# Kernel optimization log

Hardware: AMD Instinct MI355X
Metric: run time of the kernel (lower is better)

Reference implementation:

```python
import jax, jax.numpy as jnp
import numpy as np

NUM_HEADS = 16

def setup_inputs() -> dict:
    key = jax.random.key(0)
    ks = jax.random.split(key, 6)
    d_in, d_out = 1024, 1024
    x = jax.random.normal(ks[0], (4, 2048, d_in), dtype=jnp.float32)
    s = 0.02
    Wq = jax.random.normal(ks[1], (d_in, d_out), dtype=jnp.float32) * s
    Wk = jax.random.normal(ks[2], (d_in, d_out), dtype=jnp.float32) * s
    Wv = jax.random.normal(ks[3], (d_in, d_out), dtype=jnp.float32) * s
    Wo = jax.random.normal(ks[4], (d_out, d_out), dtype=jnp.float32) * s
    bo = jnp.zeros((d_out,), dtype=jnp.float32)
    return {"x": x, "Wq": Wq, "Wk": Wk, "Wv": Wv, "Wo": Wo, "bo": bo}

def reference(x, Wq, Wk, Wv, Wo, bo):
    b, n, _ = x.shape
    h = NUM_HEADS
    hd = Wq.shape[1] // h
    # project and split heads: [b, h, n, hd]
    def split(t):
        return t.reshape(b, n, h, hd).transpose(0, 2, 1, 3)
    q = split(x @ Wq)
    k = split(x @ Wk)
    v = split(x @ Wv)
    scores = jnp.einsum('bhqd,bhkd->bhqk', q, k)
    causal = jnp.tril(jnp.ones((n, n), dtype=bool))  # True = keep
    scores = jnp.where(causal, scores, -jnp.inf)
    att = jax.nn.softmax(scores / jnp.sqrt(jnp.float32(hd)), axis=-1)
    out = jnp.einsum('bhqk,bhkd->bhqd', att, v)
    out = out.transpose(0, 2, 1, 3).reshape(b, n, h * hd)
    return out @ Wo + bo
```

## Files before the change

kernel.cpp:

```cpp
#include <hip/hip_runtime.h>
#include <math.h>

namespace {
constexpr int NB = 4;
constexpr int NS = 2048;
constexpr int DM = 1024;
constexpr int NH = 16;
constexpr int DH = 64;
constexpr int M  = NB * NS;

typedef __bf16 bf16x8 __attribute__((ext_vector_type(8)));
typedef float  floatx4 __attribute__((ext_vector_type(4)));

__device__ __forceinline__ ushort f2bf(float f) {
    uint u = __float_as_uint(f);
    return (ushort)((u + 0x7FFFu + ((u >> 16) & 1u)) >> 16);
}
__device__ __forceinline__ uint cvt_pk_bf16(float lo, float hi) {
    uint r;
    asm("v_cvt_pk_bf16_f32 %0, %1, %2" : "=v"(r) : "v"(lo), "v"(hi));
    return r;
}
__device__ __forceinline__ void gload16(const void* g, void* l) {
    __builtin_amdgcn_global_load_lds(
        (const __attribute__((address_space(1))) unsigned int*)g,
        (__attribute__((address_space(3))) unsigned int*)l, 16, 0, 0);
}

__global__ __launch_bounds__(256) void conv_x_k(const float* __restrict__ in,
                                                ushort* __restrict__ out) {
    int i = blockIdx.x * 256 + threadIdx.x;
    float4 v = ((const float4*)in)[i];
    ushort4 o;
    o.x = f2bf(v.x); o.y = f2bf(v.y); o.z = f2bf(v.z); o.w = f2bf(v.w);
    ((ushort4*)out)[i] = o;
}

__global__ __launch_bounds__(256) void conv_wt4_k(const float* __restrict__ W0,
                                                  const float* __restrict__ W1,
                                                  const float* __restrict__ W2,
                                                  const float* __restrict__ W3,
                                                  ushort* __restrict__ T0,
                                                  ushort* __restrict__ T1,
                                                  ushort* __restrict__ T2,
                                                  ushort* __restrict__ T3) {
    __shared__ float tile[64][65];
    const int z = blockIdx.z;
    const float* W = (z == 0) ? W0 : (z == 1) ? W1 : (z == 2) ? W2 : W3;
    ushort* Wt     = (z == 0) ? T0 : (z == 1) ? T1 : (z == 2) ? T2 : T3;
    const int t = threadIdx.x;
    const int k0 = blockIdx.y * 64, n0 = blockIdx.x * 64;
    #pragma unroll
    for (int i = 0; i < 16; ++i) {
        int idx = i * 256 + t, r = idx >> 6, c = idx & 63;
        tile[r][c] = W[(size_t)(k0 + r) * DM + n0 + c];
    }
    __syncthreads();
    #pragma unroll
    for (int i = 0; i < 16; ++i) {
        int idx = i * 256 + t, r = idx >> 6, c = idx & 63;
        Wt[(size_t)(n0 + r) * DM + k0 + c] = f2bf(tile[c][r]);
    }
}

template<int MODE>
__global__ __launch_bounds__(512) void mm_bf16_k(const ushort* __restrict__ A,
                                                 const ushort* __restrict__ Bt,
                                                 const float* __restrict__ bias,
                                                 void* __restrict__ outp,
                                                 float oscale) {
    __shared__ __align__(16) ushort As[2 * 128 * 32];
    __shared__ __align__(16) ushort Bs[2 * 128 * 32];
    const int t  = threadIdx.x;
    const int l  = t & 63;
    const int w  = t >> 6;
    const int wr = w >> 2, wc = w & 3;
    const int lr = l & 15, lg = l >> 4;
    const int row0 = blockIdx.y * 128;
    const int col0 = blockIdx.x * 128;

    const int sr = t >> 2, scb = (t & 3) * 16;

    floatx4 acc[4][2];
    #pragma unroll
    for (int m = 0; m < 4; ++m)
        #pragma unroll
        for (int n = 0; n < 2; ++n) acc[m][n] = (floatx4){0.f, 0.f, 0.f, 0.f};

    gload16((const char*)A  + (size_t)(row0 + sr) * 2048 + scb,
            (char*)As + t * 16);
    gload16((const char*)Bt + (size_t)(col0 + sr) * 2048 + scb,
            (char*)Bs + t * 16);
    int cur = 0;

    for (int k0 = 0; k0 < DM; k0 += 32) {
        __syncthreads();
        if (k0 + 32 < DM) {
            const int nb = cur ^ 1;
            gload16((const char*)A  + (size_t)(row0 + sr) * 2048 + (size_t)(k0 + 32) * 2 + scb,
                    (char*)As + nb * 8192 + t * 16);
            gload16((const char*)Bt + (size_t)(col0 + sr) * 2048 + (size_t)(k0 + 32) * 2 + scb,
                    (char*)Bs + nb * 8192 + t * 16);
        }

        const ushort* abase = As + cur * 4096 + (wr * 64 + lr) * 32 + lg * 8;
        const ushort* bbase = Bs + cur * 4096 + (wc * 32 + lr) * 32 + lg * 8;
        bf16x8 af[4], bfv[2];
        #pragma unroll
        for (int m = 0; m < 4; ++m)
            af[m] = *(const bf16x8*)(abase + m * 16 * 32);
        #pragma unroll
        for (int n = 0; n < 2; ++n)
            bfv[n] = *(const bf16x8*)(bbase + n * 16 * 32);
        #pragma unroll
        for (int m = 0; m < 4; ++m)
            #pragma unroll
            for (int n = 0; n < 2; ++n)
                acc[m][n] = __builtin_amdgcn_mfma_f32_16x16x32_bf16(
                    af[m], bfv[n], acc[m][n], 0, 0, 0);
        cur ^= 1;
    }

    #pragma unroll
    for (int m = 0; m < 4; ++m) {
        #pragma unroll
        for (int n = 0; n < 2; ++n) {
            floatx4 d = acc[m][n];
            #pragma unroll
            for (int r = 0; r < 4; ++r) {
                int grow = row0 + wr * 64 + m * 16 + lg * 4 + r;
                int gcol = col0 + wc * 32 + n * 16 + lr;
                if (MODE == 1) {
                    ((float*)outp)[(size_t)grow * DM + gcol] = d[r] + bias[gcol];
                } else if (MODE == 2) {
                    int h = grow >> 6,  dd = grow & 63;
                    int b = gcol >> 11, nn = gcol & (NS - 1);
                    int k6 = nn & 63;
                    int np = (nn & ~63) | (k6 & 3) | (((k6 >> 5) & 1) << 2) |
                             (((k6 >> 2) & 3) << 3) | (((k6 >> 4) & 1) << 5);
                    ((ushort*)outp)[((size_t)(b * NH + h) * DH + dd) * NS + np] = f2bf(d[r]);
                } else {
                    int which = gcol >> 10;
                    int col = gcol & 1023;
                    int b = grow >> 11, nn = grow & (NS - 1);
                    int h = col >> 6,  dd = col & 63;
                    float sc = which ? 1.f : oscale;
                    ((ushort*)outp)[(size_t)which * M * DM +
                        (((size_t)(b * NH + h)) * NS + nn) * DH + dd] = f2bf(d[r] * sc);
                }
            }
        }
    }
}

__global__ __launch_bounds__(256, 4) void attn_k(const ushort* __restrict__ Q,
                                                 const ushort* __restrict__ K,
                                                 const ushort* __restrict__ Vt,
                                                 ushort* __restrict__ O) {
    __shared__ __align__(16) ushort K_lds[2 * 64 * 64];
    __shared__ __align__(16) ushort V_lds[2 * 64 * 64];

    const int t    = threadIdx.x;
    const int w    = t >> 6;
    const int l    = t & 63;
    const int lr   = l & 15;
    const int lg   = l >> 4;
    const int bh   = blockIdx.x;
    const int qblk = 31 - blockIdx.y;
    const size_t base = (size_t)bh * NS * DH;
    const int b = bh >> 4, h = bh & 15;

    const int srow_lo = l >> 3;
    const int gs      = (l & 7) ^ srow_lo;

    const int qbase  = qblk * 64;
    const int qmin_w = qbase + w * 16;
    const int qn     = qmin_w + lr;
    const int ntiles = qblk + 1;

    bf16x8 qb[2];
    #pragma unroll
    for (int kk2 = 0; kk2 < 2; ++kk2)
        qb[kk2] = *(const bf16x8*)&Q[base + (size_t)qn * DH + kk2 * 32 + lg * 8];

    uint4 ones_u = make_uint4(0x3F803F80u, 0x3F803F80u, 0x3F803F80u, 0x3F803F80u);
    bf16x8 ones_b = *(const bf16x8*)&ones_u;

    floatx4 acc[4];
    #pragma unroll
    for (int nd = 0; nd < 4; ++nd) acc[nd] = (floatx4){0.f, 0.f, 0.f, 0.f};
    floatx4 accl = (floatx4){0.f, 0.f, 0.f, 0.f};
    const floatx4 z4 = (floatx4){0.f, 0.f, 0.f, 0.f};

    #pragma unroll
    for (int i = 0; i < 2; ++i) {
        int cc = w + i * 4, rr = cc * 8 + srow_lo;
        gload16((const char*)(K + base + (size_t)rr * DH) + gs * 16,
                (char*)K_lds + cc * 1024 + l * 16);
        gload16((const char*)(Vt + base + (size_t)rr * NS) + gs * 16,
                (char*)V_lds + cc * 1024 + l * 16);
    }
    int cur = 0;

    for (int tile = 0; tile < ntiles; ++tile) {
        const int kv0 = tile * 64;
        __syncthreads();
        if (tile + 1 < ntiles) {
            const int kvn = kv0 + 64;
            const int nb = cur ^ 1;
            #pragma unroll
            for (int i = 0; i < 2; ++i) {
                int cc = w + i * 4, rr = cc * 8 + srow_lo;
                gload16((const char*)(K + base + (size_t)(kvn + rr) * DH) + gs * 16,
                        (char*)K_lds + nb * 8192 + cc * 1024 + l * 16);
                gload16((const char*)(Vt + base + (size_t)rr * NS + kvn) + gs * 16,
                        (char*)V_lds + nb * 8192 + cc * 1024 + l * 16);
            }
        }

        floatx4 s[4];
        __builtin_amdgcn_s_setprio(1);
        {
            bf16x8 ka[4];
            #pragma unroll
            for (int m = 0; m < 4; ++m)
                ka[m] = *(const bf16x8*)((const char*)K_lds + cur * 8192 +
                    (m * 16 + lr) * 128 + ((lg ^ (lr & 7)) * 16));
            #pragma unroll
            for (int m = 0; m < 4; ++m)
                s[m] = __builtin_amdgcn_mfma_f32_16x16x32_bf16(ka[m], qb[0], z4, 0, 0, 0);
            #pragma unroll
            for (int m = 0; m < 4; ++m)
                ka[m] = *(const bf16x8*)((const char*)K_lds + cur * 8192 +
                    (m * 16 + lr) * 128 + (((4 + lg) ^ (lr & 7)) * 16));
            #pragma unroll
            for (int m = 0; m < 4; ++m)
                s[m] = __builtin_amdgcn_mfma_f32_16x16x32_bf16(ka[m], qb[1], s[m], 0, 0, 0);
        }
        __builtin_amdgcn_s_setprio(0);

        const bool need_mask = (kv0 + 63 > qmin_w);
        const int kb0 = kv0 + lg * 4;
        #pragma unroll
        for (int m = 0; m < 4; ++m) {
            #pragma unroll
            for (int r = 0; r < 4; ++r) {
                float v = s[m][r];
                if (need_mask)
                    v = ((kb0 + m * 16 + r) > qn) ? -INFINITY : v;
                s[m][r] = exp2f(v);
            }
        }

        __builtin_amdgcn_s_setprio(1);
        #pragma unroll
        for (int kk2 = 0; kk2 < 2; ++kk2) {
            const int m0 = kk2, m1 = kk2 + 2;
            bf16x8 vb[4];
            #pragma unroll
            for (int nd = 0; nd < 4; ++nd)
                vb[nd] = *(const bf16x8*)((const char*)V_lds + cur * 8192 +
                    (nd * 16 + lr) * 128 + (((kk2 * 4 + lg) ^ (lr & 7)) * 16));
            uint4 pk;
            pk.x = cvt_pk_bf16(s[m0][0], s[m0][1]);
            pk.y = cvt_pk_bf16(s[m0][2], s[m0][3]);
            pk.z = cvt_pk_bf16(s[m1][0], s[m1][1]);
            pk.w = cvt_pk_bf16(s[m1][2], s[m1][3]);
            bf16x8 pa = *(const bf16x8*)&pk;
            #pragma unroll
            for (int nd = 0; nd < 4; ++nd)
                acc[nd] = __builtin_amdgcn_mfma_f32_16x16x32_bf16(
                    pa, vb[nd], acc[nd], 0, 0, 0);
            accl = __builtin_amdgcn_mfma_f32_16x16x32_bf16(
                pa, ones_b, accl, 0, 0, 0);
        }
        __builtin_amdgcn_s_setprio(0);
        cur ^= 1;
    }

    #pragma unroll
    for (int r = 0; r < 4; ++r) {
        float inv = 1.f / accl[r];
        int q = qbase + w * 16 + lg * 4 + r;
        ushort* op = &O[((size_t)(b * NS + q)) * DM + h * DH + lr];
        op[0]  = f2bf(acc[0][r] * inv);
        op[16] = f2bf(acc[1][r] * inv);
        op[32] = f2bf(acc[2][r] * inv);
        op[48] = f2bf(acc[3][r] * inv);
    }
}

}

extern "C" void kernel_launch(void* const* d_in, const int* in_sizes, int n_in,
                              void* d_out, int out_size, void* d_ws, size_t ws_size,
                              hipStream_t stream) {
    const float* x  = (const float*)d_in[0];
    const float* Wq = (const float*)d_in[1];
    const float* Wk = (const float*)d_in[2];
    const float* Wv = (const float*)d_in[3];
    const float* Wo = (const float*)d_in[4];
    const float* bo = (const float*)d_in[5];
    float* out = (float*)d_out;

    ushort* xb  = (ushort*)d_ws;
    ushort* WqT = xb  + (size_t)M * DM;
    ushort* WkT = WqT + (size_t)DM * DM;
    ushort* WvT = WkT + (size_t)DM * DM;
    ushort* WoT = WvT + (size_t)DM * DM;
    ushort* Qb  = WoT + (size_t)DM * DM;
    ushort* Kb  = Qb  + (size_t)M * DM;
    ushort* Vtg = Kb  + (size_t)M * DM;
    ushort* Ab  = Vtg + (size_t)M * DM;

    const float SCALE_Q = 0.125f * 1.4426950408889634f;

    conv_x_k<<<M * DM / 4 / 256, 256, 0, stream>>>(x, xb);
    conv_wt4_k<<<dim3(DM / 64, DM / 64, 4), 256, 0, stream>>>(
        Wq, Wk, Wv, Wo, WqT, WkT, WvT, WoT);

    mm_bf16_k<3><<<dim3(2048 / 128, M / 128), 512, 0, stream>>>(xb, WqT, nullptr, Qb, SCALE_Q);
    mm_bf16_k<2><<<dim3(M / 128, DM / 128), 512, 0, stream>>>(WvT, xb, nullptr, Vtg, 1.f);
    attn_k<<<dim3(NB * NH, 32), 256, 0, stream>>>(Qb, Kb, Vtg, Ab);
    mm_bf16_k<1><<<dim3(DM / 128, M / 128), 512, 0, stream>>>(Ab, WoT, bo, out, 1.f);
}
```

Before: 184.2 us.

## Double attention query tile per block to reuse K/V tiles across more rows

Each attention block now handles 128 query rows (32 per wave, two 16-row MFMA sub-tiles) instead of 64, so each K/V tile loaded into LDS feeds twice as many MFMAs. Grid y is halved, and waves whose rows lie entirely above the causal diagonal skip compute on that tile. exp2f is replaced with the hardware exp2 builtin. In exchange, register pressure and the number of blocks both change, which may reduce occupancy and parallelism.

```diff
diff --git a/kernel.cpp b/kernel.cpp
--- a/kernel.cpp
+++ b/kernel.cpp
@@ -20,6 +20,13 @@
     uint r;
     asm("v_cvt_pk_bf16_f32 %0, %1, %2" : "=v"(r) : "v"(lo), "v"(hi));
     return r;
+}
+__device__ __forceinline__ float fast_exp2(float x) {
+#if __has_builtin(__builtin_amdgcn_exp2f)
+    return __builtin_amdgcn_exp2f(x);
+#else
+    return exp2f(x);
+#endif
 }
 __device__ __forceinline__ void gload16(const void* g, void* l) {
     __builtin_amdgcn_global_load_lds(
@@ -166,30 +173,37 @@
     const int lr   = l & 15;
     const int lg   = l >> 4;
     const int bh   = blockIdx.x;
-    const int qblk = 31 - blockIdx.y;
+    const int qblk = 15 - blockIdx.y;
     const size_t base = (size_t)bh * NS * DH;
     const int b = bh >> 4, h = bh & 15;
 
     const int srow_lo = l >> 3;
     const int gs      = (l & 7) ^ srow_lo;
 
-    const int qbase  = qblk * 64;
-    const int qmin_w = qbase + w * 16;
-    const int qn     = qmin_w + lr;
-    const int ntiles = qblk + 1;
-
-    bf16x8 qb[2];
-    #pragma unroll
-    for (int kk2 = 0; kk2 < 2; ++kk2)
-        qb[kk2] = *(const bf16x8*)&Q[base + (size_t)qn * DH + kk2 * 32 + lg * 8];
+    const int qbase  = qblk * 128;
+    const int qmin_w = qbase + w * 32;
+    const int qmax_w = qmin_w + 31;
+    const int ntiles = 2 * (qblk + 1);
+
+    bf16x8 qb[2][2];
+    #pragma unroll
+    for (int nq = 0; nq < 2; ++nq)
+        #pragma unroll
+        for (int kk2 = 0; kk2 < 2; ++kk2)
+            qb[nq][kk2] = *(const bf16x8*)&Q[base +
+                (size_t)(qbase + w * 32 + nq * 16 + lr) * DH + kk2 * 32 + lg * 8];
 
     uint4 ones_u = make_uint4(0x3F803F80u, 0x3F803F80u, 0x3F803F80u, 0x3F803F80u);
     bf16x8 ones_b = *(const bf16x8*)&ones_u;
 
-    floatx4 acc[4];
-    #pragma unroll
-    for (int nd = 0; nd < 4; ++nd) acc[nd] = (floatx4){0.f, 0.f, 0.f, 0.f};
-    floatx4 accl = (floatx4){0.f, 0.f, 0.f, 0.f};
+    floatx4 acc[2][4];
+    #pragma unroll
+    for (int nq = 0; nq < 2; ++nq)
+        #pragma unroll
+        for (int nd = 0; nd < 4; ++nd) acc[nq][nd] = (floatx4){0.f, 0.f, 0.f, 0.f};
+    floatx4 accl[2];
+    accl[0] = (floatx4){0.f, 0.f, 0.f, 0.f};
+    accl[1] = (floatx4){0.f, 0.f, 0.f, 0.f};
     const floatx4 z4 = (floatx4){0.f, 0.f, 0.f, 0.f};
 
     #pragma unroll
@@ -218,75 +232,93 @@
             }
         }
 
-        floatx4 s[4];
-        __builtin_amdgcn_s_setprio(1);
-        {
-            bf16x8 ka[4];
-            #pragma unroll
-            for (int m = 0; m < 4; ++m)
-                ka[m] = *(const bf16x8*)((const char*)K_lds + cur * 8192 +
-                    (m * 16 + lr) * 128 + ((lg ^ (lr & 7)) * 16));
-            #pragma unroll
-            for (int m = 0; m < 4; ++m)
-                s[m] = __builtin_amdgcn_mfma_f32_16x16x32_bf16(ka[m], qb[0], z4, 0, 0, 0);
-            #pragma unroll
-            for (int m = 0; m < 4; ++m)
-                ka[m] = *(const bf16x8*)((const char*)K_lds + cur * 8192 +
-                    (m * 16 + lr) * 128 + (((4 + lg) ^ (lr & 7)) * 16));
-            #pragma unroll
-            for (int m = 0; m < 4; ++m)
-                s[m] = __builtin_amdgcn_mfma_f32_16x16x32_bf16(ka[m], qb[1], s[m], 0, 0, 0);
-        }
-        __builtin_amdgcn_s_setprio(0);
-
-        const bool need_mask = (kv0 + 63 > qmin_w);
-        const int kb0 = kv0 + lg * 4;
-        #pragma unroll
-        for (int m = 0; m < 4; ++m) {
-            #pragma unroll
-            for (int r = 0; r < 4; ++r) {
-                float v = s[m][r];
-                if (need_mask)
-                    v = ((kb0 + m * 16 + r) > qn) ? -INFINITY : v;
-                s[m][r] = exp2f(v);
-            }
-        }
-
-        __builtin_amdgcn_s_setprio(1);
-        #pragma unroll
-        for (int kk2 = 0; kk2 < 2; ++kk2) {
-            const int m0 = kk2, m1 = kk2 + 2;
-            bf16x8 vb[4];
-            #pragma unroll
-            for (int nd = 0; nd < 4; ++nd)
-                vb[nd] = *(const bf16x8*)((const char*)V_lds + cur * 8192 +
-                    (nd * 16 + lr) * 128 + (((kk2 * 4 + lg) ^ (lr & 7)) * 16));
-            uint4 pk;
-            pk.x = cvt_pk_bf16(s[m0][0], s[m0][1]);
-            pk.y = cvt_pk_bf16(s[m0][2], s[m0][3]);
-            pk.z = cvt_pk_bf16(s[m1][0], s[m1][1]);
-            pk.w = cvt_pk_bf16(s[m1][2], s[m1][3]);
-            bf16x8 pa = *(const bf16x8*)&pk;
-            #pragma unroll
-            for (int nd = 0; nd < 4; ++nd)
-                acc[nd] = __builtin_amdgcn_mfma_f32_16x16x32_bf16(
-                    pa, vb[nd], acc[nd], 0, 0, 0);
-            accl = __builtin_amdgcn_mfma_f32_16x16x32_bf16(
-                pa, ones_b, accl, 0, 0, 0);
-        }
-        __builtin_amdgcn_s_setprio(0);
+        if (kv0 <= qmax_w) {
+            floatx4 s[4][2];
+            __builtin_amdgcn_s_setprio(1);
+            {
+                bf16x8 ka[4];
+                #pragma unroll
+                for (int m = 0; m < 4; ++m)
+                    ka[m] = *(const bf16x8*)((const char*)K_lds + cur * 8192 +
+                        (m * 16 + lr) * 128 + ((lg ^ (lr & 7)) * 16));
+                #pragma unroll
+                for (int m = 0; m < 4; ++m)
+                    #pragma unroll
+                    for (int nq = 0; nq < 2; ++nq)
+                        s[m][nq] = __builtin_amdgcn_mfma_f32_16x16x32_bf16(
+                            ka[m], qb[nq][0], z4, 0, 0, 0);
+                #pragma unroll
+                for (int m = 0; m < 4; ++m)
+                    ka[m] = *(const bf16x8*)((const char*)K_lds + cur * 8192 +
+                        (m * 16 + lr) * 128 + (((4 + lg) ^ (lr & 7)) * 16));
+                #pragma unroll
+                for (int m = 0; m < 4; ++m)
+                    #pragma unroll
+                    for (int nq = 0; nq < 2; ++nq)
+                        s[m][nq] = __builtin_amdgcn_mfma_f32_16x16x32_bf16(
+                            ka[m], qb[nq][1], s[m][nq], 0, 0, 0);
+            }
+            __builtin_amdgcn_s_setprio(0);
+
+            const bool need_mask = (kv0 + 63 > qmin_w);
+            const int kb0 = kv0 + lg * 4;
+            #pragma unroll
+            for (int nq = 0; nq < 2; ++nq) {
+                const int qn = qmin_w + nq * 16 + lr;
+                #pragma unroll
+                for (int m = 0; m < 4; ++m) {
+                    #pragma unroll
+                    for (int r = 0; r < 4; ++r) {
+                        float v = s[m][nq][r];
+                        if (need_mask)
+                            v = ((kb0 + m * 16 + r) > qn) ? -INFINITY : v;
+                        s[m][nq][r] = fast_exp2(v);
+                    }
+                }
+            }
+
+            __builtin_amdgcn_s_setprio(1);
+            #pragma unroll
+            for (int kk2 = 0; kk2 < 2; ++kk2) {
+                const int m0 = kk2, m1 = kk2 + 2;
+                bf16x8 vb[4];
+                #pragma unroll
+                for (int nd = 0; nd < 4; ++nd)
+                    vb[nd] = *(const bf16x8*)((const char*)V_lds + cur * 8192 +
+                        (nd * 16 + lr) * 128 + (((kk2 * 4 + lg) ^ (lr & 7)) * 16));
+                #pragma unroll
+                for (int nq = 0; nq < 2; ++nq) {
+                    uint4 pk;
+                    pk.x = cvt_pk_bf16(s[m0][nq][0], s[m0][nq][1]);
+                    pk.y = cvt_pk_bf16(s[m0][nq][2], s[m0][nq][3]);
+                    pk.z = cvt_pk_bf16(s[m1][nq][0], s[m1][nq][1]);
+                    pk.w = cvt_pk_bf16(s[m1][nq][2], s[m1][nq][3]);
+                    bf16x8 pa = *(const bf16x8*)&pk;
+                    #pragma unroll
+                    for (int nd = 0; nd < 4; ++nd)
+                        acc[nq][nd] = __builtin_amdgcn_mfma_f32_16x16x32_bf16(
+                            pa, vb[nd], acc[nq][nd], 0, 0, 0);
+                    accl[nq] = __builtin_amdgcn_mfma_f32_16x16x32_bf16(
+                        pa, ones_b, accl[nq], 0, 0, 0);
+                }
+            }
+            __builtin_amdgcn_s_setprio(0);
+        }
         cur ^= 1;
     }
 
     #pragma unroll
-    for (int r = 0; r < 4; ++r) {
-        float inv = 1.f / accl[r];
-        int q = qbase + w * 16 + lg * 4 + r;
-        ushort* op = &O[((size_t)(b * NS + q)) * DM + h * DH + lr];
-        op[0]  = f2bf(acc[0][r] * inv);
-        op[16] = f2bf(acc[1][r] * inv);
-        op[32] = f2bf(acc[2][r] * inv);
-        op[48] = f2bf(acc[3][r] * inv);
+    for (int nq = 0; nq < 2; ++nq) {
+        #pragma unroll
+        for (int r = 0; r < 4; ++r) {
+            float inv = 1.f / accl[nq][r];
+            int q = qbase + w * 32 + nq * 16 + lg * 4 + r;
+            ushort* op = &O[((size_t)(b * NS + q)) * DM + h * DH + lr];
+            op[0]  = f2bf(acc[nq][0][r] * inv);
+            op[16] = f2bf(acc[nq][1][r] * inv);
+            op[32] = f2bf(acc[nq][2][r] * inv);
+            op[48] = f2bf(acc[nq][3][r] * inv);
+        }
     }
 }
 
@@ -321,6 +353,6 @@
 
     mm_bf16_k<3><<<dim3(2048 / 128, M / 128), 512, 0, stream>>>(xb, WqT, nullptr, Qb, SCALE_Q);
     mm_bf16_k<2><<<dim3(M / 128, DM / 128), 512, 0, stream>>>(WvT, xb, nullptr, Vtg, 1.f);
-    attn_k<<<dim3(NB * NH, 32), 256, 0, stream>>>(Qb, Kb, Vtg, Ab);
+    attn_k<<<dim3(NB * NH, 16), 256, 0, stream>>>(Qb, Kb, Vtg, Ab);
     mm_bf16_k<1><<<dim3(DM / 128, M / 128), 512, 0, stream>>>(Ab, WoT, bo, out, 1.f);
 }
```

New measurement: 175.6 us. 1.05x faster.
